# Kernel optimization log

Measured on AMD Instinct MI355X. Metric: run time of the kernel, lower is better.

The kernel has to match this reference:

```python
import jax, jax.numpy as jnp
import numpy as np
from jax import lax

RATIOS = (0.5, 1.0, 2.0)
SCALES = (8, 16, 32)
BASE = 16
STRIDE = 16
N_PRE = 6000
N_POST = 300      # post-NMS proposals kept
NMS_THRESH = 0.7
MIN_SIZE = 16.0


def _anchor_base():
    x = y = BASE / 2.0
    ab = np.zeros((len(RATIOS) * len(SCALES), 4), np.float32)
    for i, r in enumerate(RATIOS):
        for j, s in enumerate(SCALES):
            h = BASE * s * np.sqrt(r)
            w = BASE * s * np.sqrt(1.0 / r)
            k = i * len(SCALES) + j
            ab[k] = [y - h / 2, x - w / 2, y + h / 2, x + w / 2]
    return ab


def _anchors(h, w):
    ab = _anchor_base()
    sy = np.arange(0, h * STRIDE, STRIDE)
    sx = np.arange(0, w * STRIDE, STRIDE)
    sx, sy = np.meshgrid(sx, sy)
    shift = np.stack((sy.ravel(), sx.ravel(), sy.ravel(), sx.ravel()), axis=1)
    # [K, A, 4] -> [K*A, 4], row-major over (y, x) pixels matching NHWC flatten
    return (ab[None, :, :] + shift[:, None, :]).reshape(-1, 4).astype(np.float32)


def _conv(x, w, b, pad):
    y = lax.conv_general_dilated(x, w, (1, 1), ((pad, pad), (pad, pad)),
                                 dimension_numbers=('NCHW', 'OIHW', 'NCHW'))
    return y + b[None, :, None, None]


def _loc2bbox(anchor, loc):
    h = anchor[:, 2] - anchor[:, 0]
    w = anchor[:, 3] - anchor[:, 1]
    cy = anchor[:, 0] + 0.5 * h
    cx = anchor[:, 1] + 0.5 * w
    dy, dx, dh, dw = loc[:, 0], loc[:, 1], loc[:, 2], loc[:, 3]
    ncy = dy * h + cy
    ncx = dx * w + cx
    nh = jnp.exp(dh) * h
    nw = jnp.exp(dw) * w
    return jnp.stack([ncy - 0.5 * nh, ncx - 0.5 * nw, ncy + 0.5 * nh, ncx + 0.5 * nw], axis=1)


def _iou(b):
    tl = jnp.maximum(b[:, None, :2], b[None, :, :2])
    br = jnp.minimum(b[:, None, 2:], b[None, :, 2:])
    wh = jnp.clip(br - tl, 0.0)
    inter = wh[..., 0] * wh[..., 1]
    area = (b[:, 2] - b[:, 0]) * (b[:, 3] - b[:, 1])
    return inter / (area[:, None] + area[None, :] - inter + 1e-9)


def _nms_keep(iou):
    # greedy NMS over score-sorted boxes: suppress later boxes overlapping kept earlier ones
    n = iou.shape[0]
    idx = jnp.arange(n)
    def step(keep, i):
        sup = (iou[i] > NMS_THRESH) & (idx > i) & keep[i]
        return keep & (~sup), None
    keep, _ = lax.scan(step, jnp.ones((n,), dtype=bool), idx)
    return keep


def _proposal(loc, fg, anchor, img_h, img_w, scale=1.0):
    boxes = _loc2bbox(anchor, loc)
    boxes = jnp.stack([jnp.clip(boxes[:, 0], 0.0, img_h),
                       jnp.clip(boxes[:, 1], 0.0, img_w),
                       jnp.clip(boxes[:, 2], 0.0, img_h),
                       jnp.clip(boxes[:, 3], 0.0, img_w)], axis=1)
    hs = boxes[:, 2] - boxes[:, 0]
    ws = boxes[:, 3] - boxes[:, 1]
    ms = MIN_SIZE * scale
    score = jnp.where((hs >= ms) & (ws >= ms), fg, -jnp.inf)
    top, idx = lax.top_k(score, N_PRE)
    bk = boxes[idx]                                    # [N_PRE, 4]
    keep = _nms_keep(_iou(lax.stop_gradient(bk)))      # selection is non-differentiable
    fs = jnp.where(keep, top, -jnp.inf)
    _, o2 = lax.top_k(fs, N_POST)
    return bk[o2]                                      # [N_POST, 4]


def setup_inputs() -> dict:
    key = jax.random.key(0)
    ks = jax.random.split(key, 4)
    C, H, W = 512, 50, 76
    return {
        "feature": jax.random.normal(ks[0], (1, C, H, W), jnp.float32),
        "conv1_w": jax.random.normal(ks[1], (512, C, 3, 3), jnp.float32) * 0.01,
        "conv1_b": jnp.zeros((512,), jnp.float32),
        "score_w": jax.random.normal(ks[2], (18, 512, 1, 1), jnp.float32) * 0.01,
        "score_b": jnp.zeros((18,), jnp.float32),
        "loc_w": jax.random.normal(ks[3], (36, 512, 1, 1), jnp.float32) * 0.01,
        "loc_b": jnp.zeros((36,), jnp.float32),
        "img_h": 800,
        "img_w": 1216,
    }


def reference(feature, conv1_w, conv1_b, score_w, score_b, loc_w, loc_b, img_h, img_w):
    _, c, h, w = feature.shape
    A = 9
    anchor = jnp.asarray(_anchors(h, w))
    x = jax.nn.relu(_conv(feature, conv1_w, conv1_b, 1))
    locs = _conv(x, loc_w, loc_b, 0)
    rpn_locs = locs.transpose(0, 2, 3, 1).reshape(1, -1, 4)
    sc = _conv(x, score_w, score_b, 0).transpose(0, 2, 3, 1)   # [1, h, w, 2A]
    sm = jax.nn.softmax(sc.reshape(1, h, w, A, 2), axis=-1)
    fg = sm[..., 1].reshape(-1)
    rpn_scores = sc.reshape(1, -1, 2)
    rois = _proposal(rpn_locs[0], fg, anchor, float(img_h), float(img_w), scale=1.0)
    return rpn_locs, rpn_scores, rois, anchor
```

## Files before the change

kernel.cpp:

```cpp
#include <hip/hip_runtime.h>

#define HH 50
#define WW2 76
#define NPIX 3800
#define CIN 512
#define NANCH 34200
#define NPRE 6000
#define NPOST 300
#define WPR 94

typedef unsigned long long u64;
typedef unsigned int u32;

__device__ __forceinline__ int PADL(int i) { return i + (i >> 4); }

template <bool DOW>
__global__ __launch_bounds__(256) void rpn_wtrans(const float* __restrict__ wgt,
                                                  float* __restrict__ wt,
                                                  const float* __restrict__ sw,
                                                  const float* __restrict__ lw,
                                                  float* __restrict__ wt2,
                                                  u32* __restrict__ hist,
                                                  u32* __restrict__ info) {
    __shared__ float tile[32][33];
    const int bx = blockIdx.x;
    const int by = blockIdx.y;
    const int t  = threadIdx.x;
    const int tx = t & 31, ty = t >> 5;
    int gid = (by * 144 + bx) * 256 + t;
    if (gid < 65536) hist[gid] = 0u;
    else if (gid < 65552) info[gid - 65536] = 0u;
    if (gid < 32768) {
        int c = gid >> 6, n = gid & 63;
        float v = 0.f;
        if (n < 18) v = sw[n * 512 + c];
        else if (n < 54) v = lw[(n - 18) * 512 + c];
        wt2[((c >> 2) * 64 + n) * 4 + (c & 3)] = v;
    }
    if (!DOW) return;
#pragma unroll
    for (int r = 0; r < 32; r += 8) {
        int ko = by * 32 + ty + r;
        tile[ty + r][tx] = wgt[(size_t)ko * 4608 + bx * 32 + tx];
    }
    __syncthreads();
#pragma unroll
    for (int r = 0; r < 32; r += 8) {
        int cit = bx * 32 + ty + r;
        wt[(size_t)cit * 512 + by * 32 + tx] = tile[tx][ty + r];
    }
}

template <bool USEWT>
__global__ __launch_bounds__(256, 2) void rpn_conv1(
    const float* __restrict__ feat, const float* __restrict__ wsrc,
    float* __restrict__ Xpt, int cin_blk) {
    const int yb = blockIdx.x;
    const int kg = blockIdx.y;
    const int cz = blockIdx.z;
    const int t  = threadIdx.x;
    const int kp = t & 15;
    const int ty = t >> 4;
    const int row  = ty >> 2;
    const int xseg = ty & 3;
    const int x0 = xseg * 19;
    __shared__ float in_l[2048];
    __shared__ float w_l[2304];

    const int y0 = yb * 4 - 1;
    int inSrc[8]; u32 inValid = 0, inPad = 0;
#pragma unroll
    for (int k = 0; k < 8; ++k) {
        int q = t + k * 256;
        int c = q / 504, rem = q - c * 504;
        int r = rem / 84, xx = rem - r * 84;
        int gy = y0 + r, gx = xx - 1;
        bool inb = q < 2016;
        bool ok = inb && ((unsigned)gy < 50u) && ((unsigned)gx < 76u);
        inSrc[k] = c * NPIX + gy * 76 + gx;
        if (ok) inValid |= (1u << k);
        else if (inb) inPad |= (1u << k);
    }
#pragma unroll
    for (int k = 0; k < 8; ++k)
        if ((inPad >> k) & 1) in_l[t + k * 256] = 0.f;

    const float* wb;
    int wOffA = 0;
    int wSrc[9];
    if (USEWT) {
        wb = wsrc + (size_t)(cz * cin_blk) * 9 * 512 + kg * 64;
        wOffA = 8 * t - 7 * (t & 63);
    } else {
        wb = wsrc + (size_t)(kg * 64) * 4608 + (size_t)(cz * cin_blk) * 9;
#pragma unroll
        for (int k = 0; k < 9; ++k) {
            int q = t + k * 256;
            int c = q / 576, r2 = q - c * 576;
            int tap = r2 >> 6, ko = r2 & 63;
            wSrc[k] = ko * 4608 + c * 9 + tap;
        }
    }

    const float* fb = feat + (size_t)(cz * cin_blk) * NPIX;
    float acc[4][19];
#pragma unroll
    for (int o = 0; o < 4; ++o)
#pragma unroll
        for (int p = 0; p < 19; ++p) acc[o][p] = 0.f;

    const int niter = cin_blk >> 2;
#pragma unroll 1
    for (int it = 0; it < niter; ++it) {
        __syncthreads();
#pragma unroll
        for (int k = 0; k < 8; ++k)
            if ((inValid >> k) & 1) in_l[t + k * 256] = fb[inSrc[k]];
        if (USEWT) {
#pragma unroll
            for (int k = 0; k < 9; ++k)
                w_l[t + k * 256] = wb[wOffA + k * 2048];
        } else {
#pragma unroll
            for (int k = 0; k < 9; ++k)
                w_l[t + k * 256] = wb[wSrc[k]];
        }
        __syncthreads();
#pragma unroll 1
        for (int c = 0; c < 4; ++c) {
            const float* ir0 = &in_l[(c * 6 + row) * 84 + x0];
            const float* wl  = &w_l[c * 576 + 4 * kp];
#pragma unroll
            for (int r = 0; r < 3; ++r) {
                const float* ir = ir0 + r * 84;
                float win[21];
#pragma unroll
                for (int w = 0; w < 21; ++w) win[w] = ir[w];
                float wv[4][3];
#pragma unroll
                for (int tp = 0; tp < 3; ++tp) {
                    const float* wr = wl + (r * 3 + tp) * 64;
#pragma unroll
                    for (int o = 0; o < 4; ++o) wv[o][tp] = wr[o];
                }
#pragma unroll
                for (int p = 0; p < 19; ++p) {
#pragma unroll
                    for (int o = 0; o < 4; ++o) {
                        acc[o][p] = fmaf(wv[o][0], win[p],     acc[o][p]);
                        acc[o][p] = fmaf(wv[o][1], win[p + 1], acc[o][p]);
                        acc[o][p] = fmaf(wv[o][2], win[p + 2], acc[o][p]);
                    }
                }
            }
        }
        fb += 4 * NPIX;
        wb += USEWT ? 4 * 9 * 512 : 36;
    }

    const int k0 = kg * 64 + 4 * kp;
    const int y = yb * 4 + row;
    if (y < 50) {
        float* d0 = Xpt + ((size_t)cz * NPIX + y * 76 + x0) * 512 + k0;
#pragma unroll
        for (int p = 0; p < 19; ++p)
            *reinterpret_cast<float4*>(d0 + (size_t)p * 512) =
                make_float4(acc[0][p], acc[1][p], acc[2][p], acc[3][p]);
    }
}

__global__ __launch_bounds__(64) void rpn_head(
    const float* __restrict__ Xpt, const float* __restrict__ wt2,
    const float* __restrict__ b1,
    const float* __restrict__ sb, const float* __restrict__ lb,
    const int* __restrict__ ihp, const int* __restrict__ iwp,
    float* __restrict__ out, float* __restrict__ boxes,
    u32* __restrict__ keys, u32* __restrict__ hist, int nz) {
    const int p0 = blockIdx.x * 8;
    const int t  = threadIdx.x;
    __shared__ __align__(16) float xs[8 * 512];
    __shared__ float ovl[8][64];
    float4* dst = reinterpret_cast<float4*>(xs);
#pragma unroll
    for (int i = 0; i < 16; ++i) {
        int idx = t + i * 64;
        int px = idx >> 7, cc = idx & 127;
        float4 v = *reinterpret_cast<const float4*>(b1 + cc * 4);
        const float* src = Xpt + ((size_t)(p0 + px)) * 512 + cc * 4;
        for (int z = 0; z < nz; ++z) {
            float4 x = *reinterpret_cast<const float4*>(src + (size_t)z * NPIX * 512);
            v.x += x.x; v.y += x.y; v.z += x.z; v.w += x.w;
        }
        v.x = fmaxf(v.x, 0.f); v.y = fmaxf(v.y, 0.f);
        v.z = fmaxf(v.z, 0.f); v.w = fmaxf(v.w, 0.f);
        dst[idx] = v;
    }
    __syncthreads();
    float acc[8];
    {
        float b = (t < 18) ? sb[t] : ((t < 54) ? lb[t - 18] : 0.f);
#pragma unroll
        for (int px = 0; px < 8; ++px) acc[px] = b;
    }
    const float4* wv = reinterpret_cast<const float4*>(wt2) + t;
#pragma unroll 4
    for (int c4 = 0; c4 < 128; ++c4) {
        float4 w = wv[c4 * 64];
#pragma unroll
        for (int px = 0; px < 8; ++px) {
            float4 x = *reinterpret_cast<const float4*>(xs + px * 512 + c4 * 4);
            acc[px] = fmaf(w.x, x.x, acc[px]);
            acc[px] = fmaf(w.y, x.y, acc[px]);
            acc[px] = fmaf(w.z, x.z, acc[px]);
            acc[px] = fmaf(w.w, x.w, acc[px]);
        }
    }
#pragma unroll
    for (int px = 0; px < 8; ++px) ovl[px][t] = acc[px];
    __syncthreads();
    const float ch = (float)(*ihp), cw = (float)(*iwp);
#pragma unroll
    for (int pass = 0; pass < 2; ++pass) {
        int a, px;
        bool act;
        if (pass == 0) { act = (t < 63); px = t / 9; a = t - px * 9; }
        else           { act = (t < 9);  px = 7;     a = t; }
        if (act) {
            const int p = p0 + px;
            const float* ov = ovl[px];
            const float s0 = ov[2 * a], s1 = ov[2 * a + 1];
            const float dy = ov[18 + 4 * a], dx = ov[18 + 4 * a + 1];
            const float dh = ov[18 + 4 * a + 2], dw = ov[18 + 4 * a + 3];
            const int yy = p / WW2, xx = p % WW2;
            const int ai = p * 9 + a;
            *reinterpret_cast<float4*>(out + ai * 4) = make_float4(dy, dx, dh, dw);
            *reinterpret_cast<float2*>(out + 136800 + ai * 2) = make_float2(s0, s1);
            double r  = (a < 3) ? 0.5 : (a < 6) ? 1.0 : 2.0;
            int m3 = a % 3;
            double s2 = (m3 == 0) ? 8.0 : (m3 == 1) ? 16.0 : 32.0;
            double hd = (16.0 * s2) * sqrt(r);
            double wd = (16.0 * s2) * sqrt(1.0 / r);
            float ay1 = (float)(8.0 - hd * 0.5), ax1 = (float)(8.0 - wd * 0.5);
            float ay2 = (float)(8.0 + hd * 0.5), ax2 = (float)(8.0 + wd * 0.5);
            float fy = (float)(yy * 16), fx = (float)(xx * 16);
            float A0 = ay1 + fy, A1 = ax1 + fx, A2 = ay2 + fy, A3 = ax2 + fx;
            *reinterpret_cast<float4*>(out + 206400 + ai * 4) = make_float4(A0, A1, A2, A3);
            float ah = __fsub_rn(A2, A0), aw = __fsub_rn(A3, A1);
            float cy = __fadd_rn(A0, __fmul_rn(0.5f, ah));
            float cx = __fadd_rn(A1, __fmul_rn(0.5f, aw));
            float ncy = __fadd_rn(__fmul_rn(dy, ah), cy);
            float ncx = __fadd_rn(__fmul_rn(dx, aw), cx);
            float nh = __fmul_rn(expf(dh), ah);
            float nw = __fmul_rn(expf(dw), aw);
            float b0 = __fsub_rn(ncy, __fmul_rn(0.5f, nh));
            float b1v = __fsub_rn(ncx, __fmul_rn(0.5f, nw));
            float b2 = __fadd_rn(ncy, __fmul_rn(0.5f, nh));
            float b3 = __fadd_rn(ncx, __fmul_rn(0.5f, nw));
            b0 = fminf(fmaxf(b0, 0.f), ch); b2 = fminf(fmaxf(b2, 0.f), ch);
            b1v = fminf(fmaxf(b1v, 0.f), cw); b3 = fminf(fmaxf(b3, 0.f), cw);
            float hs = __fsub_rn(b2, b0), wsz = __fsub_rn(b3, b1v);
            float m = fmaxf(s0, s1);
            float e0 = expf(__fsub_rn(s0, m)), e1 = expf(__fsub_rn(s1, m));
            float fg = __fdiv_rn(e1, __fadd_rn(e0, e1));
            float score = (hs >= 16.f && wsz >= 16.f) ? fg : -__builtin_inff();
            *reinterpret_cast<float4*>(boxes + ai * 4) = make_float4(b0, b1v, b2, b3);
            u32 kb = __float_as_uint(score);
            kb = (kb & 0x80000000u) ? ~kb : (kb | 0x80000000u);
            keys[ai] = kb;
            atomicAdd(&hist[kb >> 16], 1u);
        }
    }
}

__global__ __launch_bounds__(1024) void rpn_topk(const u32* __restrict__ hist,
                                                 const u32* __restrict__ keys,
                                                 const float* __restrict__ boxes,
                                                 float* __restrict__ bk) {
    __shared__ u64 s[8704];
    __shared__ u32 part[256], h2[256];
    __shared__ int segs;
    __shared__ u32 Tsh, cnt;
    const int t = threadIdx.x;
    if (t == 0) cnt = 0u;
    u32* tmp = (u32*)s;
    {
        u32 sum = 0;
        const u32* hp = hist + t * 64;
#pragma unroll 8
        for (int b = 0; b < 64; ++b) sum += hp[b];
        tmp[t] = sum;
    }
    __syncthreads();
    u32 p4 = 0;
    if (t < 256) p4 = tmp[4 * t] + tmp[4 * t + 1] + tmp[4 * t + 2] + tmp[4 * t + 3];
    __syncthreads();
    if (t < 256) part[t] = p4;
    __syncthreads();
    for (int off = 1; off < 256; off <<= 1) {
        u32 v = 0, add = 0;
        if (t < 256) { v = part[t]; add = (t + off < 256) ? part[t + off] : 0u; }
        __syncthreads();
        if (t < 256) part[t] = v + add;
        __syncthreads();
    }
    if (t < 256) {
        u32 suf  = part[t];
        u32 sufn = (t < 255) ? part[t + 1] : 0u;
        if (suf >= NPRE && sufn < NPRE) segs = t;
    }
    __syncthreads();
    const int seg = segs;
    const u32 above = (seg < 255) ? part[seg + 1] : 0u;
    if (t < 256) h2[t] = hist[seg * 256 + t];
    __syncthreads();
    for (int off = 1; off < 256; off <<= 1) {
        u32 v = 0, add = 0;
        if (t < 256) { v = h2[t]; add = (t + off < 256) ? h2[t + off] : 0u; }
        __syncthreads();
        if (t < 256) h2[t] = v + add;
        __syncthreads();
    }
    if (t < 256) {
        u32 tot  = above + h2[t];
        u32 totn = above + ((t < 255) ? h2[t + 1] : 0u);
        if (tot >= NPRE && totn < NPRE) Tsh = (u32)(seg * 256 + t);
    }
    __syncthreads();
    const u32 T = Tsh;
    const int lane = t & 63;
    for (int base = 0; base < NANCH; base += 1024) {
        int idx = base + t;
        u32 k = (idx < NANCH) ? keys[idx] : 0u;
        bool sel = (idx < NANCH) && ((k >> 16) >= T);
        u64 ball = __ballot(sel);
        u32 wbase = 0;
        if (lane == 0 && ball) wbase = atomicAdd(&cnt, (u32)__popcll(ball));
        wbase = __shfl(wbase, 0);
        if (sel) {
            u32 pos = wbase + (u32)__popcll(ball & ((1ull << lane) - 1ull));
            if (pos < 8192) s[PADL((int)pos)] = ((u64)k << 32) | (u64)(0xFFFFFFFFu - (u32)idx);
        }
    }
    __syncthreads();
    {
        int n = (int)cnt; if (n > 8192) n = 8192;
        for (int i = t; i < 8192; i += 1024)
            if (i >= n) s[PADL(i)] = 0ull;
    }
    __syncthreads();
    for (int k = 2; k <= 8192; k <<= 1) {
        for (int j = k >> 1; j > 0; j >>= 1) {
#pragma unroll 4
            for (int z = 0; z < 4; ++z) {
                int pi = t + z * 1024;
                int p1 = ((pi & ~(j - 1)) << 1) | (pi & (j - 1));
                int p2 = p1 | j;
                bool desc = ((p1 & k) == 0);
                u64 A = s[PADL(p1)], B = s[PADL(p2)];
                if (desc ? (A < B) : (A > B)) { s[PADL(p1)] = B; s[PADL(p2)] = A; }
            }
            __syncthreads();
        }
    }
    for (int i = t; i < NPRE; i += 1024) {
        u32 oi = 0xFFFFFFFFu - (u32)(s[PADL(i)] & 0xFFFFFFFFull);
        if (oi >= NANCH) oi = 0;
        reinterpret_cast<float4*>(bk)[i] = reinterpret_cast<const float4*>(boxes)[oi];
    }
}

__global__ __launch_bounds__(64) void rpn_iou(const float* __restrict__ bk,
                                              u64* __restrict__ mask) {
    const int t = threadIdx.x;
    const int bj = blockIdx.x, bi = blockIdx.y;
    const int j0 = bj * 64;
    const int i = bi * 64 + t;
    if (j0 + 63 <= bi * 64) {
        if (i < NPRE) mask[(size_t)i * WPR + bj] = 0ull;
        return;
    }
    __shared__ float4 jb[64];
    jb[t] = (j0 + t < NPRE) ? reinterpret_cast<const float4*>(bk)[j0 + t]
                            : make_float4(0.f, 0.f, 0.f, 0.f);
    __syncthreads();
    if (i >= NPRE) return;
    float4 b = reinterpret_cast<const float4*>(bk)[i];
    float areai = __fmul_rn(__fsub_rn(b.z, b.x), __fsub_rn(b.w, b.y));
    u64 bits = 0ull;
    for (int jj = 0; jj < 64; ++jj) {
        int j = j0 + jj;
        if (j <= i || j >= NPRE) continue;
        float4 c = jb[jj];
        float ty = fmaxf(b.x, c.x), tx = fmaxf(b.y, c.y);
        float by = fminf(b.z, c.z), bx2 = fminf(b.w, c.w);
        float ih = fmaxf(__fsub_rn(by, ty), 0.f);
        float iw = fmaxf(__fsub_rn(bx2, tx), 0.f);
        float inter = __fmul_rn(ih, iw);
        float areaj = __fmul_rn(__fsub_rn(c.z, c.x), __fsub_rn(c.w, c.y));
        float denom = __fadd_rn(__fsub_rn(__fadd_rn(areai, areaj), inter), 1e-9f);
        float iou = __fdiv_rn(inter, denom);
        if (iou > 0.7f) bits |= (1ull << jj);
    }
    mask[(size_t)i * WPR + bj] = bits;
}

__global__ __launch_bounds__(64) void rpn_nms(const u64* __restrict__ mask,
                                              const float* __restrict__ bk,
                                              float* __restrict__ rois) {
    const int lane = threadIdx.x;
    u64 rem0 = 0ull, rem1 = 0ull, curW = 0ull;
    __shared__ unsigned short klist[304];
    int kcnt = 0;
    u64 pm0[16], pm1[16], pmg[16];
#pragma unroll
    for (int u = 0; u < 16; ++u) {
        pm0[u] = mask[(size_t)u * WPR + lane];
        pm1[u] = (lane < 30) ? mask[(size_t)u * WPR + 64 + lane] : 0ull;
        pmg[u] = mask[(size_t)u * WPR + 0];
    }
    bool done = false;
    for (int base = 0; base < NPRE && !done; base += 16) {
        if ((base & 63) == 0) {
            int w = base >> 6;
            curW = (w < 64) ? __shfl(rem0, w) : __shfl(rem1, w - 64);
        }
#pragma unroll
        for (int u = 0; u < 16; ++u) {
            const int i = base + u;
            u64 m0 = pm0[u], m1 = pm1[u], mg = pmg[u];
            const int ni = i + 16;
            pm0[u] = mask[(size_t)ni * WPR + lane];
            pm1[u] = (lane < 30) ? mask[(size_t)ni * WPR + 64 + lane] : 0ull;
            pmg[u] = mask[(size_t)ni * WPR + (ni >> 6)];
            if (((curW >> (i & 63)) & 1ull) == 0ull) {
                rem0 |= m0;
                rem1 |= m1;
                curW |= mg;
                if (lane == 0 && kcnt < 304) klist[kcnt] = (unsigned short)i;
                ++kcnt;
                if (kcnt >= NPOST) { done = true; break; }
            }
        }
    }
    __syncthreads();
    const int nk = kcnt < NPOST ? kcnt : NPOST;
    for (int r = lane; r < nk; r += 64) {
        int bi = klist[r];
        reinterpret_cast<float4*>(rois)[r] = reinterpret_cast<const float4*>(bk)[bi];
    }
    if (kcnt < NPOST) {
        int pos = kcnt;
        for (int i = 0; i < NPRE && pos < NPOST; ++i) {
            int w = i >> 6;
            u64 wv = (w < 64) ? __shfl(rem0, w) : __shfl(rem1, w - 64);
            if ((wv >> (i & 63)) & 1ull) {
                if (lane < 4) rois[pos * 4 + lane] = bk[i * 4 + lane];
                ++pos;
            }
        }
    }
}

extern "C" void kernel_launch(void* const* d_in, const int* in_sizes, int n_in,
                              void* d_out, int out_size, void* d_ws, size_t ws_size,
                              hipStream_t stream) {
    (void)in_sizes; (void)n_in; (void)out_size;
    const float* feat = (const float*)d_in[0];
    const float* w1   = (const float*)d_in[1];
    const float* b1   = (const float*)d_in[2];
    const float* sw   = (const float*)d_in[3];
    const float* sb   = (const float*)d_in[4];
    const float* lw   = (const float*)d_in[5];
    const float* lb   = (const float*)d_in[6];
    const int*   ih   = (const int*)d_in[7];
    const int*   iw   = (const int*)d_in[8];
    float* out = (float*)d_out;

    const size_t WT_B    = 9437184;
    const size_t WT2_B   = 131072;
    const size_t REST_B  = WT2_B + 547200 + 136800 + 262144 + 64 + 96000 + 4528128;
    const size_t SLICE_B = (size_t)512 * NPIX * 4;
    int nz; bool usewt;
    if      (ws_size >= 8 * SLICE_B + WT_B + REST_B) { nz = 8; usewt = true; }
    else if (ws_size >= 4 * SLICE_B + WT_B + REST_B) { nz = 4; usewt = true; }
    else if (ws_size >= 2 * SLICE_B + WT_B + REST_B) { nz = 2; usewt = true; }
    else                                             { nz = 2; usewt = false; }

    char* p = (char*)d_ws;
    float* Xpt = (float*)p;          p += (size_t)nz * SLICE_B;
    float* wt = nullptr;
    if (usewt) { wt = (float*)p;     p += WT_B; }
    float* wt2    = (float*)p;       p += WT2_B;
    float* boxes  = (float*)p;       p += 547200;
    u32*   keys   = (u32*)p;         p += 136800;
    u32*   hist   = (u32*)p;         p += 262144;
    u32*   info   = (u32*)p;         p += 64;
    float* bk     = (float*)p;       p += 96000;
    u64*   mask   = (u64*)p;

    const int cin_blk = 512 / nz;

    if (usewt) {
        rpn_wtrans<true><<<dim3(144, 16), 256, 0, stream>>>(w1, wt, sw, lw, wt2, hist, info);
        rpn_conv1<true><<<dim3(13, 8, nz), 256, 0, stream>>>(feat, wt, Xpt, cin_blk);
    } else {
        rpn_wtrans<false><<<dim3(144, 16), 256, 0, stream>>>(w1, nullptr, sw, lw, wt2, hist, info);
        rpn_conv1<false><<<dim3(13, 8, nz), 256, 0, stream>>>(feat, w1, Xpt, cin_blk);
    }
    rpn_head<<<475, 64, 0, stream>>>(Xpt, wt2, b1, sb, lb, ih, iw, out, boxes, keys, hist, nz);
    rpn_topk<<<1, 1024, 0, stream>>>(hist, keys, boxes, bk);
    rpn_iou<<<dim3(WPR, WPR), 64, 0, stream>>>(bk, mask);
    rpn_nms<<<1, 64, 0, stream>>>(mask, bk, out + 205200);
}
```

Baseline: 623.9 us.

## Split top-k bitonic sort across blocks and launch conv1 in two halves

The single-block top-k kernel is replaced by a pipeline of kernels. One block picks the threshold and compacts the candidates into a global buffer. Four blocks each sort a 2048-element segment in LDS, then global compare-exchange passes and LDS merge kernels finish the 8192-element bitonic sort, and the last merge gathers the pre-NMS boxes. The goal is to spread the long serial sort over more compute units, at the cost of several extra kernel launches and global-memory round trips. Separately, the conv1 launch is split into two launches over halves of the channel-slice dimension.

```diff
diff --git a/kernel.cpp b/kernel.cpp
--- a/kernel.cpp
+++ b/kernel.cpp
@@ -54,10 +54,10 @@
 template <bool USEWT>
 __global__ __launch_bounds__(256, 2) void rpn_conv1(
     const float* __restrict__ feat, const float* __restrict__ wsrc,
-    float* __restrict__ Xpt, int cin_blk) {
+    float* __restrict__ Xpt, int cin_blk, int czbase) {
     const int yb = blockIdx.x;
     const int kg = blockIdx.y;
-    const int cz = blockIdx.z;
+    const int cz = blockIdx.z + czbase;
     const int t  = threadIdx.x;
     const int kp = t & 15;
     const int ty = t >> 4;
@@ -272,29 +272,24 @@
     }
 }
 
-__global__ __launch_bounds__(1024) void rpn_topk(const u32* __restrict__ hist,
-                                                 const u32* __restrict__ keys,
-                                                 const float* __restrict__ boxes,
-                                                 float* __restrict__ bk) {
-    __shared__ u64 s[8704];
+__global__ __launch_bounds__(1024) void rpn_threshsel(const u32* __restrict__ hist,
+                                                      u32* __restrict__ info,
+                                                      const u32* __restrict__ keys,
+                                                      u64* __restrict__ selk) {
+    __shared__ u32 tmp[1024];
     __shared__ u32 part[256], h2[256];
     __shared__ int segs;
-    __shared__ u32 Tsh, cnt;
+    __shared__ u32 Tsh;
     const int t = threadIdx.x;
-    if (t == 0) cnt = 0u;
-    u32* tmp = (u32*)s;
     {
-        u32 sum = 0;
+        u32 s = 0;
         const u32* hp = hist + t * 64;
 #pragma unroll 8
-        for (int b = 0; b < 64; ++b) sum += hp[b];
-        tmp[t] = sum;
-    }
-    __syncthreads();
-    u32 p4 = 0;
-    if (t < 256) p4 = tmp[4 * t] + tmp[4 * t + 1] + tmp[4 * t + 2] + tmp[4 * t + 3];
-    __syncthreads();
-    if (t < 256) part[t] = p4;
+        for (int b = 0; b < 64; ++b) s += hp[b];
+        tmp[t] = s;
+    }
+    __syncthreads();
+    if (t < 256) part[t] = tmp[4 * t] + tmp[4 * t + 1] + tmp[4 * t + 2] + tmp[4 * t + 3];
     __syncthreads();
     for (int off = 1; off < 256; off <<= 1) {
         u32 v = 0, add = 0;
@@ -334,38 +329,77 @@
         bool sel = (idx < NANCH) && ((k >> 16) >= T);
         u64 ball = __ballot(sel);
         u32 wbase = 0;
-        if (lane == 0 && ball) wbase = atomicAdd(&cnt, (u32)__popcll(ball));
+        if (lane == 0 && ball) wbase = atomicAdd(&info[2], (u32)__popcll(ball));
         wbase = __shfl(wbase, 0);
         if (sel) {
             u32 pos = wbase + (u32)__popcll(ball & ((1ull << lane) - 1ull));
-            if (pos < 8192) s[PADL((int)pos)] = ((u64)k << 32) | (u64)(0xFFFFFFFFu - (u32)idx);
-        }
-    }
-    __syncthreads();
-    {
-        int n = (int)cnt; if (n > 8192) n = 8192;
-        for (int i = t; i < 8192; i += 1024)
-            if (i >= n) s[PADL(i)] = 0ull;
-    }
-    __syncthreads();
-    for (int k = 2; k <= 8192; k <<= 1) {
+            if (pos < 8192) selk[pos] = ((u64)k << 32) | (u64)(0xFFFFFFFFu - (u32)idx);
+        }
+    }
+}
+
+__global__ __launch_bounds__(1024) void rpn_sort_local(u64* __restrict__ selk,
+                                                       const u32* __restrict__ info) {
+    __shared__ u64 s[2176];
+    const int t = threadIdx.x;
+    const int seg = blockIdx.x;
+    const int base = seg * 2048;
+    int n = (int)info[2]; if (n > 8192) n = 8192;
+    for (int i = t; i < 2048; i += 1024)
+        s[PADL(i)] = (base + i < n) ? selk[base + i] : 0ull;
+    __syncthreads();
+    const bool D = ((seg & 1) == 0);
+    for (int k = 2; k <= 2048; k <<= 1) {
         for (int j = k >> 1; j > 0; j >>= 1) {
-#pragma unroll 4
-            for (int z = 0; z < 4; ++z) {
-                int pi = t + z * 1024;
-                int p1 = ((pi & ~(j - 1)) << 1) | (pi & (j - 1));
-                int p2 = p1 | j;
-                bool desc = ((p1 & k) == 0);
-                u64 A = s[PADL(p1)], B = s[PADL(p2)];
-                if (desc ? (A < B) : (A > B)) { s[PADL(p1)] = B; s[PADL(p2)] = A; }
+            int p1 = ((t & ~(j - 1)) << 1) | (t & (j - 1));
+            int p2 = p1 | j;
+            bool desc = (((p1 & k) == 0) == D);
+            u64 A = s[PADL(p1)], B = s[PADL(p2)];
+            if (desc ? (A < B) : (A > B)) { s[PADL(p1)] = B; s[PADL(p2)] = A; }
+            __syncthreads();
+        }
+    }
+    for (int i = t; i < 2048; i += 1024) selk[base + i] = s[PADL(i)];
+}
+
+__global__ __launch_bounds__(512) void rpn_sort_gpass(u64* __restrict__ selk,
+                                                      int k, int j) {
+    int i = blockIdx.x * 512 + threadIdx.x;
+    int p1 = ((i & ~(j - 1)) << 1) | (i & (j - 1));
+    int p2 = p1 | j;
+    bool desc = ((p1 & k) == 0);
+    u64 A = selk[p1], B = selk[p2];
+    if (desc ? (A < B) : (A > B)) { selk[p1] = B; selk[p2] = A; }
+}
+
+template <bool FINAL>
+__global__ __launch_bounds__(1024) void rpn_sort_lmerge(u64* __restrict__ selk, int k,
+                                                        const float* __restrict__ boxes,
+                                                        float* __restrict__ bk) {
+    __shared__ u64 s[2176];
+    const int t = threadIdx.x;
+    const int base = blockIdx.x * 2048;
+    for (int i = t; i < 2048; i += 1024) s[PADL(i)] = selk[base + i];
+    __syncthreads();
+    const bool desc = ((base & k) == 0);
+    for (int j = 1024; j > 0; j >>= 1) {
+        int p1 = ((t & ~(j - 1)) << 1) | (t & (j - 1));
+        int p2 = p1 | j;
+        u64 A = s[PADL(p1)], B = s[PADL(p2)];
+        if (desc ? (A < B) : (A > B)) { s[PADL(p1)] = B; s[PADL(p2)] = A; }
+        __syncthreads();
+    }
+    if (FINAL) {
+        for (int i = t; i < 2048; i += 1024) {
+            int r = base + i;
+            if (r < NPRE) {
+                u32 oi = 0xFFFFFFFFu - (u32)(s[PADL(i)] & 0xFFFFFFFFull);
+                if (oi >= NANCH) oi = 0;
+                reinterpret_cast<float4*>(bk)[r] = reinterpret_cast<const float4*>(boxes)[oi];
             }
-            __syncthreads();
-        }
-    }
-    for (int i = t; i < NPRE; i += 1024) {
-        u32 oi = 0xFFFFFFFFu - (u32)(s[PADL(i)] & 0xFFFFFFFFull);
-        if (oi >= NANCH) oi = 0;
-        reinterpret_cast<float4*>(bk)[i] = reinterpret_cast<const float4*>(boxes)[oi];
+        }
+    } else {
+        for (int i = t; i < 2048; i += 1024) selk[base + i] = s[PADL(i)];
     }
 }
 
@@ -478,7 +512,7 @@
 
     const size_t WT_B    = 9437184;
     const size_t WT2_B   = 131072;
-    const size_t REST_B  = WT2_B + 547200 + 136800 + 262144 + 64 + 96000 + 4528128;
+    const size_t REST_B  = WT2_B + 547200 + 136800 + 262144 + 64 + 65536 + 96000 + 4528128;
     const size_t SLICE_B = (size_t)512 * NPIX * 4;
     int nz; bool usewt;
     if      (ws_size >= 8 * SLICE_B + WT_B + REST_B) { nz = 8; usewt = true; }
@@ -495,20 +529,30 @@
     u32*   keys   = (u32*)p;         p += 136800;
     u32*   hist   = (u32*)p;         p += 262144;
     u32*   info   = (u32*)p;         p += 64;
+    u64*   selk   = (u64*)p;         p += 65536;
     float* bk     = (float*)p;       p += 96000;
     u64*   mask   = (u64*)p;
 
     const int cin_blk = 512 / nz;
+    const int half = nz / 2;
 
     if (usewt) {
         rpn_wtrans<true><<<dim3(144, 16), 256, 0, stream>>>(w1, wt, sw, lw, wt2, hist, info);
-        rpn_conv1<true><<<dim3(13, 8, nz), 256, 0, stream>>>(feat, wt, Xpt, cin_blk);
+        rpn_conv1<true><<<dim3(13, 8, half), 256, 0, stream>>>(feat, wt, Xpt, cin_blk, 0);
+        rpn_conv1<true><<<dim3(13, 8, nz - half), 256, 0, stream>>>(feat, wt, Xpt, cin_blk, half);
     } else {
         rpn_wtrans<false><<<dim3(144, 16), 256, 0, stream>>>(w1, nullptr, sw, lw, wt2, hist, info);
-        rpn_conv1<false><<<dim3(13, 8, nz), 256, 0, stream>>>(feat, w1, Xpt, cin_blk);
+        rpn_conv1<false><<<dim3(13, 8, half), 256, 0, stream>>>(feat, w1, Xpt, cin_blk, 0);
+        rpn_conv1<false><<<dim3(13, 8, nz - half), 256, 0, stream>>>(feat, w1, Xpt, cin_blk, half);
     }
     rpn_head<<<475, 64, 0, stream>>>(Xpt, wt2, b1, sb, lb, ih, iw, out, boxes, keys, hist, nz);
-    rpn_topk<<<1, 1024, 0, stream>>>(hist, keys, boxes, bk);
+    rpn_threshsel<<<1, 1024, 0, stream>>>(hist, info, keys, selk);
+    rpn_sort_local<<<4, 1024, 0, stream>>>(selk, info);
+    rpn_sort_gpass<<<8, 512, 0, stream>>>(selk, 4096, 2048);
+    rpn_sort_lmerge<false><<<4, 1024, 0, stream>>>(selk, 4096, nullptr, nullptr);
+    rpn_sort_gpass<<<8, 512, 0, stream>>>(selk, 8192, 4096);
+    rpn_sort_gpass<<<8, 512, 0, stream>>>(selk, 8192, 2048);
+    rpn_sort_lmerge<true><<<4, 1024, 0, stream>>>(selk, 8192, boxes, bk);
     rpn_iou<<<dim3(WPR, WPR), 64, 0, stream>>>(bk, mask);
     rpn_nms<<<1, 64, 0, stream>>>(mask, bk, out + 205200);
 }
```

After: 613.0 us. Within noise of the previous version (-1.8%).
